# Optimization experiments

Hardware: AMD Instinct MI355X
Metric: run time of the kernel (lower is better)

Reference implementation:

```python
import jax, jax.numpy as jnp
import numpy as np

B, M, A = 64, 16, 128
H = 128            # cfg.SUB.DIM
P = 16             # NUM_PHYSICOCHEMICAL
NUM_ATOM_TYPES = 100
NUM_FP_TYPES = 2048
EPS_W = 1e-8
EPS_LN = 1e-5


def setup_inputs() -> dict:
    key = jax.random.key(0)
    ks = jax.random.split(key, 16)
    def xavier(k, shape):
        fan_in, fan_out = shape[0], shape[-1]
        lim = float(np.sqrt(6.0 / (fan_in + fan_out)))
        return jax.random.uniform(k, shape, jnp.float32, -lim, lim)
    return {
        "atom_features": jax.random.randint(ks[0], (B, M, A), 0, NUM_ATOM_TYPES),
        "fingerprints": jax.random.randint(ks[1], (B, M, A), 0, NUM_FP_TYPES),
        "phys": jax.random.normal(ks[2], (B, M, P), jnp.float32),
        "ratios": jax.random.uniform(ks[3], (B, M), jnp.float32),
        # learned params
        "atom_emb": xavier(ks[4], (NUM_ATOM_TYPES, H)),
        "fp_emb": xavier(ks[5], (NUM_FP_TYPES, H)),
        "W_in": xavier(ks[6], (2 * H, H)),
        "b_in": jnp.zeros((H,), jnp.float32),
        "ln_g": jnp.ones((H + P,), jnp.float32),
        "ln_b": jnp.zeros((H + P,), jnp.float32),
        "W1": xavier(ks[7], (H + P, H)),
        "b1": jnp.zeros((H,), jnp.float32),
        "W2": xavier(ks[8], (H, 1)),
        "b2": jnp.zeros((1,), jnp.float32),
    }


def reference(atom_features, fingerprints, phys, ratios,
              atom_emb, fp_emb, W_in, b_in, ln_g, ln_b, W1, b1, W2, b2):
    # per-molecule embed: gather both tables, concat, linear, relu, mean over atoms
    e = jnp.concatenate([atom_emb[atom_features], fp_emb[fingerprints]], axis=-1)  # [B,M,A,2H]
    h = jax.nn.relu(jnp.einsum('bmad,dh->bmah', e, W_in) + b_in)                   # [B,M,A,H]
    mol = h.mean(axis=2)                                                           # [B,M,H]

    pv = jnp.nan_to_num(phys, nan=0.0, posinf=1000.0, neginf=-1000.0)              # [B,M,P]

    # normalized mixing weights per batch item
    w = ratios / (ratios.sum(axis=1, keepdims=True) + EPS_W)                       # [B,M]
    mix_h = jnp.einsum('bm,bmh->bh', w, mol)                                       # [B,H]
    mix_p = jnp.einsum('bm,bmp->bp', w, pv)                                        # [B,P]

    z = jnp.concatenate([mix_h, mix_p], axis=-1)                                   # [B,H+P]
    # head: LayerNorm -> Linear -> ReLU -> Linear (dropout p=0, eval)
    mu = z.mean(axis=-1, keepdims=True)
    var = ((z - mu) ** 2).mean(axis=-1, keepdims=True)
    zn = (z - mu) / jnp.sqrt(var + EPS_LN) * ln_g + ln_b
    y = jax.nn.relu(zn @ W1 + b1) @ W2 + b2                                        # [B,1]
    return jnp.nan_to_num(y)
```

## Files before the change

kernel.cpp:

```cpp
#include <hip/hip_runtime.h>
#include <math.h>
#include <float.h>

#define B_ 64
#define M_ 16
#define A_ 128
#define H_ 128
#define P_ 16
#define NAT 100
#define NFP 2048
#define ZDIM (H_ + P_)

__device__ float g_Ta[NAT * H_];
__device__ float g_Tf[NFP * H_];
__device__ float g_mol[B_ * M_ * H_];

__global__ __launch_bounds__(128)
void k1_precompute(const float* __restrict__ atom_emb,
                   const float* __restrict__ fp_emb,
                   const float* __restrict__ W_in) {
    __shared__ float e[H_];
    const int r = blockIdx.x, j = threadIdx.x;
    const float* emb;
    const float* W;
    float* out;
    if (r < NAT) { emb = atom_emb + r * H_; W = W_in;             out = g_Ta + r * H_; }
    else { int rf = r - NAT; emb = fp_emb + rf * H_; W = W_in + H_ * H_; out = g_Tf + rf * H_; }
    e[j] = emb[j];
    __syncthreads();
    float acc = 0.f;
#pragma unroll 16
    for (int k = 0; k < H_; ++k) acc += e[k] * W[k * H_ + j];
    out[j] = acc;
}

__global__ __launch_bounds__(128)
void k2_mol(const int* __restrict__ af, const int* __restrict__ fpi,
            const float* __restrict__ b_in) {
    __shared__ int ia[A_];
    __shared__ int ifp[A_];
    const int bm = blockIdx.x, j = threadIdx.x;
    ia[j]  = af[bm * A_ + j];
    ifp[j] = fpi[bm * A_ + j];
    __syncthreads();
    const float bj = b_in[j];
    float acc = 0.f;
#pragma unroll 16
    for (int a = 0; a < A_; ++a) {
        float v = g_Ta[ia[a] * H_ + j] + g_Tf[ifp[a] * H_ + j] + bj;
        acc += fmaxf(v, 0.f);
    }
    g_mol[bm * H_ + j] = acc * (1.0f / (float)A_);
}

__global__ __launch_bounds__(128)
void k3_head(const float* __restrict__ phys,
             const float* __restrict__ ratios,
             const float* __restrict__ ln_g,
             const float* __restrict__ ln_b,
             const float* __restrict__ W1,
             const float* __restrict__ b1,
             const float* __restrict__ W2,
             const float* __restrict__ b2,
             float* __restrict__ out) {
    const int b = blockIdx.x, j = threadIdx.x;
    __shared__ float w[M_];
    __shared__ float z[ZDIM];
    __shared__ float zn[ZDIM];
    __shared__ float red[H_];

    if (j < M_) w[j] = ratios[b * M_ + j];
    __syncthreads();

    float rsum = 0.f;
#pragma unroll
    for (int m = 0; m < M_; ++m) rsum += w[m];
    const float dinv = 1.0f / (rsum + 1e-8f);

    float acc = 0.f;
#pragma unroll
    for (int m = 0; m < M_; ++m) acc += (w[m] * dinv) * g_mol[(b * M_ + m) * H_ + j];
    z[j] = acc;

    if (j < P_) {
        float accp = 0.f;
#pragma unroll
        for (int m = 0; m < M_; ++m) {
            float pv = phys[(b * M_ + m) * P_ + j];
            if (isnan(pv)) pv = 0.f;
            else if (isinf(pv)) pv = (pv > 0.f) ? 1000.f : -1000.f;
            accp += (w[m] * dinv) * pv;
        }
        z[H_ + j] = accp;
    }
    __syncthreads();

    float s = 0.f;
#pragma unroll 8
    for (int k = 0; k < ZDIM; ++k) s += z[k];
    const float mu = s * (1.0f / (float)ZDIM);
    float s2 = 0.f;
#pragma unroll 8
    for (int k = 0; k < ZDIM; ++k) { float d = z[k] - mu; s2 += d * d; }
    const float rstd = rsqrtf(s2 * (1.0f / (float)ZDIM) + 1e-5f);

    for (int k = j; k < ZDIM; k += H_)
        zn[k] = (z[k] - mu) * rstd * ln_g[k] + ln_b[k];
    __syncthreads();

    float a1 = 0.f;
#pragma unroll 8
    for (int k = 0; k < ZDIM; ++k) a1 += zn[k] * W1[k * H_ + j];
    const float h1 = fmaxf(a1 + b1[j], 0.f);
    red[j] = h1 * W2[j];
    __syncthreads();

    if (j == 0) {
        float y = b2[0];
#pragma unroll 8
        for (int k = 0; k < H_; ++k) y += red[k];
        if (isnan(y)) y = 0.f;
        else if (isinf(y)) y = (y > 0.f) ? FLT_MAX : -FLT_MAX;
        out[b] = y;
    }
}

extern "C" void kernel_launch(void* const* d_in, const int* in_sizes, int n_in,
                              void* d_out, int out_size, void* d_ws, size_t ws_size,
                              hipStream_t stream) {
    const int*   af    = (const int*)d_in[0];
    const int*   fpi   = (const int*)d_in[1];
    const float* phys  = (const float*)d_in[2];
    const float* ratio = (const float*)d_in[3];
    const float* aemb  = (const float*)d_in[4];
    const float* femb  = (const float*)d_in[5];
    const float* W_in  = (const float*)d_in[6];
    const float* b_in  = (const float*)d_in[7];
    const float* ln_g  = (const float*)d_in[8];
    const float* ln_b  = (const float*)d_in[9];
    const float* W1    = (const float*)d_in[10];
    const float* b1    = (const float*)d_in[11];
    const float* W2    = (const float*)d_in[12];
    const float* b2    = (const float*)d_in[13];
    float* out = (float*)d_out;

    k1_precompute<<<dim3(NAT + NFP), dim3(H_), 0, stream>>>(aemb, femb, W_in);
    k2_mol<<<dim3(B_ * M_), dim3(H_), 0, stream>>>(af, fpi, b_in);
    k3_head<<<dim3(B_), dim3(H_), 0, stream>>>(phys, ratio, ln_g, ln_b, W1, b1, W2, b2, out);
}
```

Measured before the change: 109.3 us.

## Reuse W_in loads across four rows in precompute and vectorise mol gather

The table-precompute kernel now computes four embedding rows per block, so each W_in element loaded from memory feeds four accumulators and the block count drops fourfold. The molecule kernel switches to float4 gathers, with each wavefront covering a subset of atoms, and a shared-memory reduction combines the four partial sums. This is meant to cut redundant weight traffic and the number of load instructions in the gather. In exchange it adds an extra barrier and shared-memory reduction in k2, and k1 launches fewer blocks (537 vs 2148), which may leave the GPU less fully occupied.

```diff
diff --git a/kernel.cpp b/kernel.cpp
--- a/kernel.cpp
+++ b/kernel.cpp
@@ -15,23 +15,35 @@
 __device__ float g_Tf[NFP * H_];
 __device__ float g_mol[B_ * M_ * H_];
 
+#define K1_BLOCKS (NAT / 4 + NFP / 4)
 __global__ __launch_bounds__(128)
 void k1_precompute(const float* __restrict__ atom_emb,
                    const float* __restrict__ fp_emb,
                    const float* __restrict__ W_in) {
-    __shared__ float e[H_];
-    const int r = blockIdx.x, j = threadIdx.x;
-    const float* emb;
-    const float* W;
-    float* out;
-    if (r < NAT) { emb = atom_emb + r * H_; W = W_in;             out = g_Ta + r * H_; }
-    else { int rf = r - NAT; emb = fp_emb + rf * H_; W = W_in + H_ * H_; out = g_Tf + rf * H_; }
-    e[j] = emb[j];
+    __shared__ float e[4][H_];
+    const int j = threadIdx.x;
+    const float* emb; const float* W; float* out; int base;
+    if (blockIdx.x < NAT / 4) {
+        base = blockIdx.x * 4;           emb = atom_emb; W = W_in;            out = g_Ta;
+    } else {
+        base = (blockIdx.x - NAT / 4) * 4; emb = fp_emb;  W = W_in + H_ * H_; out = g_Tf;
+    }
+#pragma unroll
+    for (int r = 0; r < 4; ++r) e[r][j] = emb[(base + r) * H_ + j];
     __syncthreads();
-    float acc = 0.f;
-#pragma unroll 16
-    for (int k = 0; k < H_; ++k) acc += e[k] * W[k * H_ + j];
-    out[j] = acc;
+    float a0 = 0.f, a1 = 0.f, a2 = 0.f, a3 = 0.f;
+#pragma unroll 8
+    for (int k = 0; k < H_; ++k) {
+        const float wk = W[k * H_ + j];
+        a0 += e[0][k] * wk;
+        a1 += e[1][k] * wk;
+        a2 += e[2][k] * wk;
+        a3 += e[3][k] * wk;
+    }
+    out[(base + 0) * H_ + j] = a0;
+    out[(base + 1) * H_ + j] = a1;
+    out[(base + 2) * H_ + j] = a2;
+    out[(base + 3) * H_ + j] = a3;
 }
 
 __global__ __launch_bounds__(128)
@@ -39,18 +51,29 @@
             const float* __restrict__ b_in) {
     __shared__ int ia[A_];
     __shared__ int ifp[A_];
-    const int bm = blockIdx.x, j = threadIdx.x;
-    ia[j]  = af[bm * A_ + j];
-    ifp[j] = fpi[bm * A_ + j];
+    __shared__ float sh[4][H_];
+    const int bm = blockIdx.x, t = threadIdx.x;
+    const int q = t & 31, s = t >> 5;
+    ia[t]  = af[bm * A_ + t];
+    ifp[t] = fpi[bm * A_ + t];
     __syncthreads();
-    const float bj = b_in[j];
-    float acc = 0.f;
-#pragma unroll 16
-    for (int a = 0; a < A_; ++a) {
-        float v = g_Ta[ia[a] * H_ + j] + g_Tf[ifp[a] * H_ + j] + bj;
-        acc += fmaxf(v, 0.f);
+    const float4 bj = *(const float4*)&b_in[4 * q];
+    float4 acc = make_float4(0.f, 0.f, 0.f, 0.f);
+#pragma unroll 8
+    for (int a = s; a < A_; a += 4) {
+        const int ra = ia[a], rf = ifp[a];
+        const float4 va = *(const float4*)&g_Ta[ra * H_ + 4 * q];
+        const float4 vf = *(const float4*)&g_Tf[rf * H_ + 4 * q];
+        acc.x += fmaxf(va.x + vf.x + bj.x, 0.f);
+        acc.y += fmaxf(va.y + vf.y + bj.y, 0.f);
+        acc.z += fmaxf(va.z + vf.z + bj.z, 0.f);
+        acc.w += fmaxf(va.w + vf.w + bj.w, 0.f);
     }
-    g_mol[bm * H_ + j] = acc * (1.0f / (float)A_);
+    *(float4*)&sh[s][4 * q] = acc;
+    __syncthreads();
+    const int j = t;
+    g_mol[bm * H_ + j] =
+        (sh[0][j] + sh[1][j] + sh[2][j] + sh[3][j]) * (1.0f / (float)A_);
 }
 
 __global__ __launch_bounds__(128)
@@ -144,7 +167,7 @@
     const float* b2    = (const float*)d_in[13];
     float* out = (float*)d_out;
 
-    k1_precompute<<<dim3(NAT + NFP), dim3(H_), 0, stream>>>(aemb, femb, W_in);
+    k1_precompute<<<dim3(K1_BLOCKS), dim3(H_), 0, stream>>>(aemb, femb, W_in);
     k2_mol<<<dim3(B_ * M_), dim3(H_), 0, stream>>>(af, fpi, b_in);
     k3_head<<<dim3(B_), dim3(H_), 0, stream>>>(phys, ratio, ln_g, ln_b, W1, b1, W2, b2, out);
 }
```

Result: no change. 108.0 us (-1.1%).
